# Kernel optimization log

Measured on AMD Instinct MI355X. Metric: run time of the kernel, lower is better.

The kernel has to match this reference:

```python
import jax, jax.numpy as jnp
import numpy as np

N_T, N_C, N_M = 300000, 100000, 20000
D_IN, D, D_OUT = 390, 128, 64
H_PRE, H_POST = 256, 64


def _nrm(k, shape, scale=0.02):
    return jax.random.normal(k, shape, dtype=jnp.float32) * scale


def setup_inputs() -> dict:
    key = jax.random.key(0)
    ks = jax.random.split(key, 24)
    inp = {
        'input_features': jax.random.normal(ks[0], (N_T, D_IN), jnp.float32),
        'card_of_target': jax.random.randint(ks[1], (N_T,), 0, N_C, jnp.int32),
        'merchant_of_target': jax.random.randint(ks[2], (N_T,), 0, N_M, jnp.int32),
        # HeteroEmbedding tables for src types feeding 'target'
        'card_emb': _nrm(ks[3], (N_C, D)),
        'merch_emb': _nrm(ks[4], (N_M, D)),
        # target_preprocessing FFBlock (390 -> 256 -> 128, n_layers=2)
        'pre_Wi': _nrm(ks[5], (D_IN, H_PRE)), 'pre_bi': jnp.zeros((H_PRE,), jnp.float32),
        'pre_Wh': _nrm(ks[6], (H_PRE, H_PRE)), 'pre_bh': jnp.zeros((H_PRE,), jnp.float32),
        'pre_Wo': _nrm(ks[7], (H_PRE, D)), 'pre_bo': jnp.zeros((D,), jnp.float32),
        # conv1 / conv2: one GraphConv per etype; order:
        # 0=card->target, 1=merchant->target, 2=target->card, 3=target->merchant
        'conv1_W': _nrm(ks[8], (4, D, D)), 'conv1_b': jnp.zeros((4, D), jnp.float32),
        'conv2_W': _nrm(ks[9], (4, D, D)), 'conv2_b': jnp.zeros((4, D), jnp.float32),
        # conv3: dst=='target' -> D_OUT; dst!='target' -> 1
        'conv3_Wt': _nrm(ks[10], (2, D, D_OUT)), 'conv3_bt': jnp.zeros((2, D_OUT), jnp.float32),
        'conv3_Wo': _nrm(ks[11], (2, D, 1)), 'conv3_bo': jnp.zeros((2, 1), jnp.float32),
        # target_postprocessing FFBlock (64 -> 64 -> 1, n_layers=2)
        'post_Wi': _nrm(ks[12], (D_OUT, H_POST)), 'post_bi': jnp.zeros((H_POST,), jnp.float32),
        'post_Wh': _nrm(ks[13], (H_POST, H_POST)), 'post_bh': jnp.zeros((H_POST,), jnp.float32),
        'post_Wo': _nrm(ks[14], (H_POST, 1)), 'post_bo': jnp.zeros((1,), jnp.float32),
    }
    return inp


def _ff(x, Wi, bi, Wh, bh, Wo, bo, n_layers=2):
    h = jax.nn.relu(x @ Wi + bi)
    for _ in range(1, n_layers):
        h = jax.nn.relu(h @ Wh + bh)
    return h @ Wo + bo


def _deg(ids, n):
    # degree per node over edge endpoint list, clamped to >= 1 (DGL GraphConv)
    return jnp.maximum(jnp.zeros((n,), jnp.float32).at[ids].add(1.0), 1.0)


def _gconv(x_src, src, dst, n_dst, W, b, d_src, d_dst):
    # DGL GraphConv, norm='both': scale src by out_deg^-1/2, matmul,
    # sum messages onto dst, scale by in_deg^-1/2, add bias.
    h = (x_src * jax.lax.rsqrt(d_src)[:, None]) @ W          # [n_src, out]
    agg = jax.ops.segment_sum(h[src], dst, num_segments=n_dst)
    return agg * jax.lax.rsqrt(d_dst)[:, None] + b


def reference(input_features, card_of_target, merchant_of_target,
              card_emb, merch_emb,
              pre_Wi, pre_bi, pre_Wh, pre_bh, pre_Wo, pre_bo,
              conv1_W, conv1_b, conv2_W, conv2_b,
              conv3_Wt, conv3_bt, conv3_Wo, conv3_bo,
              post_Wi, post_bi, post_Wh, post_bh, post_Wo, post_bo):
    n_t, n_c, n_m = input_features.shape[0], card_emb.shape[0], merch_emb.shape[0]
    t_ids = jnp.arange(n_t, dtype=jnp.int32)
    d_c = _deg(card_of_target, n_c)      # card degree (in/out symmetric here)
    d_m = _deg(merchant_of_target, n_m)  # merchant degree
    d_t = _deg(t_ids, n_t)               # target degree (=1 per etype)

    tf = _ff(input_features, pre_Wi, pre_bi, pre_Wh, pre_bh, pre_Wo, pre_bo)

    # conv1 (HeteroGraphConv, aggregate='sum') + relu
    h1_t = (_gconv(card_emb, card_of_target, t_ids, n_t, conv1_W[0], conv1_b[0], d_c, d_t)
            + _gconv(merch_emb, merchant_of_target, t_ids, n_t, conv1_W[1], conv1_b[1], d_m, d_t))
    h1_c = _gconv(tf, t_ids, card_of_target, n_c, conv1_W[2], conv1_b[2], d_t, d_c)
    h1_m = _gconv(tf, t_ids, merchant_of_target, n_m, conv1_W[3], conv1_b[3], d_t, d_m)
    h1_t, h1_c, h1_m = jax.nn.relu(h1_t), jax.nn.relu(h1_c), jax.nn.relu(h1_m)

    # conv2 applied (conv_layers - 2) = 1 time
    h2_t, h2_c, h2_m = h1_t, h1_c, h1_m
    for _ in range(2, 3):
        n_t2 = (_gconv(h2_c, card_of_target, t_ids, n_t, conv2_W[0], conv2_b[0], d_c, d_t)
                + _gconv(h2_m, merchant_of_target, t_ids, n_t, conv2_W[1], conv2_b[1], d_m, d_t))
        n_c2 = _gconv(h2_t, t_ids, card_of_target, n_c, conv2_W[2], conv2_b[2], d_t, d_c)
        n_m2 = _gconv(h2_t, t_ids, merchant_of_target, n_m, conv2_W[3], conv2_b[3], d_t, d_m)
        h2_t, h2_c, h2_m = jax.nn.relu(n_t2), jax.nn.relu(n_c2), jax.nn.relu(n_m2)

    # conv3: D_OUT into target, 1 into non-target dsts; no relu
    h3_t = (_gconv(h2_c, card_of_target, t_ids, n_t, conv3_Wt[0], conv3_bt[0], d_c, d_t)
            + _gconv(h2_m, merchant_of_target, t_ids, n_t, conv3_Wt[1], conv3_bt[1], d_m, d_t))
    h3_c = _gconv(h2_t, t_ids, card_of_target, n_c, conv3_Wo[0], conv3_bo[0], d_t, d_c)
    h3_m = _gconv(h2_t, t_ids, merchant_of_target, n_m, conv3_Wo[1], conv3_bo[1], d_t, d_m)

    h3_t = _ff(h3_t, post_Wi, post_bi, post_Wh, post_bh, post_Wo, post_bo)
    return h3_t, h3_c, h3_m
```

## Files before the change

### kernel.cpp

```cpp
#include <hip/hip_runtime.h>


#define NT 300000
#define NC 100000
#define NM 20000
#define DIN 390
#define DD 128
#define DOUT 64
#define HPRE 256
#define HPOST 64

typedef _Float16 half8 __attribute__((ext_vector_type(8)));
typedef float f32x16 __attribute__((ext_vector_type(16)));

#define LO_SCALE 512.0f
#define LO_INV   (1.0f / 512.0f)

__device__ __forceinline__ void split2(float x, _Float16& h, _Float16& l) {
    _Float16 hh = (_Float16)x;
    h = hh;
    l = (_Float16)((x - (float)hh) * LO_SCALE);
}

template<int TM, int TN, int WGM, int WGN>
__global__ __launch_bounds__(256, 2) void gemm_mfma(
    const float* __restrict__ A, const _Float16* __restrict__ Wh,
    const _Float16* __restrict__ Wl, const float* __restrict__ bias,
    const float* __restrict__ rowscale, float* __restrict__ C,
    int M, int K, int N, int Kpad, int relu)
{
    constexpr int BM = 32 * TM * WGM;
    constexpr int BN = 32 * TN * WGN;
    constexpr int RS = 40;
    __shared__ __align__(16) _Float16 Ah[BM * RS];
    __shared__ __align__(16) _Float16 Al[BM * RS];
    __shared__ __align__(16) _Float16 Bh[BN * RS];
    __shared__ __align__(16) _Float16 Bl[BN * RS];

    const int tid  = (int)threadIdx.x;
    const int lane = tid & 63;
    const int wave = tid >> 6;
    const int wm0 = (wave % WGM) * 32 * TM;
    const int wn0 = (wave / WGM) * 32 * TN;
    const int bm = blockIdx.x * BM;
    const int bn = blockIdx.y * BN;

    f32x16 zz;
    #pragma unroll
    for (int i = 0; i < 16; ++i) zz[i] = 0.f;
    f32x16 acc_hh[TM][TN], acc_x[TM][TN];
    #pragma unroll
    for (int tm = 0; tm < TM; ++tm)
        #pragma unroll
        for (int tn = 0; tn < TN; ++tn) { acc_hh[tm][tn] = zz; acc_x[tm][tn] = zz; }

    const int sar = tid >> 1;
    const int sak = (tid & 1) * 16;
    const int agrow = bm + sar;
    const float* Aptr = A + (size_t)agrow * K;

    const int ml  = lane & 31;
    const int klo = (lane >> 5) * 8;

    for (int k0 = 0; k0 < K; k0 += 32) {
        {
            _Float16 hh[16], ll[16];
            #pragma unroll
            for (int q = 0; q < 4; ++q) {
                const int kb = k0 + sak + q * 4;
                float4 f = make_float4(0.f, 0.f, 0.f, 0.f);
                if (agrow < M) {
                    if (kb + 3 < K) {
                        f = *(const float4*)(Aptr + kb);
                    } else {
                        if (kb + 0 < K) f.x = Aptr[kb + 0];
                        if (kb + 1 < K) f.y = Aptr[kb + 1];
                        if (kb + 2 < K) f.z = Aptr[kb + 2];
                        if (kb + 3 < K) f.w = Aptr[kb + 3];
                    }
                }
                split2(f.x, hh[q * 4 + 0], ll[q * 4 + 0]);
                split2(f.y, hh[q * 4 + 1], ll[q * 4 + 1]);
                split2(f.z, hh[q * 4 + 2], ll[q * 4 + 2]);
                split2(f.w, hh[q * 4 + 3], ll[q * 4 + 3]);
            }
            half8 h0, h1, l0, l1;
            #pragma unroll
            for (int j = 0; j < 8; ++j) {
                h0[j] = hh[j]; h1[j] = hh[8 + j];
                l0[j] = ll[j]; l1[j] = ll[8 + j];
            }
            *(half8*)&Ah[sar * RS + sak]     = h0;
            *(half8*)&Ah[sar * RS + sak + 8] = h1;
            *(half8*)&Al[sar * RS + sak]     = l0;
            *(half8*)&Al[sar * RS + sak + 8] = l1;
        }
        if constexpr (BN == 128) {
            const int n = tid >> 1, kq = (tid & 1) * 16;
            const size_t g = (size_t)(bn + n) * Kpad + k0 + kq;
            *(half8*)&Bh[n * RS + kq]     = *(const half8*)(Wh + g);
            *(half8*)&Bh[n * RS + kq + 8] = *(const half8*)(Wh + g + 8);
            *(half8*)&Bl[n * RS + kq]     = *(const half8*)(Wl + g);
            *(half8*)&Bl[n * RS + kq + 8] = *(const half8*)(Wl + g + 8);
        } else {
            const int n = tid >> 2, kq = (tid & 3) * 8;
            const size_t g = (size_t)(bn + n) * Kpad + k0 + kq;
            *(half8*)&Bh[n * RS + kq] = *(const half8*)(Wh + g);
            *(half8*)&Bl[n * RS + kq] = *(const half8*)(Wl + g);
        }
        __syncthreads();

        #pragma unroll
        for (int ks = 0; ks < 2; ++ks) {
            const int kk = ks * 16 + klo;
            half8 fa_h[TM], fa_l[TM], fb_h[TN], fb_l[TN];
            #pragma unroll
            for (int t = 0; t < TM; ++t) {
                const int m = wm0 + t * 32 + ml;
                fa_h[t] = *(const half8*)&Ah[m * RS + kk];
                fa_l[t] = *(const half8*)&Al[m * RS + kk];
            }
            #pragma unroll
            for (int t = 0; t < TN; ++t) {
                const int n = wn0 + t * 32 + ml;
                fb_h[t] = *(const half8*)&Bh[n * RS + kk];
                fb_l[t] = *(const half8*)&Bl[n * RS + kk];
            }
            #pragma unroll
            for (int tm = 0; tm < TM; ++tm)
                #pragma unroll
                for (int tn = 0; tn < TN; ++tn) {
                    acc_hh[tm][tn] = __builtin_amdgcn_mfma_f32_32x32x16_f16(
                        fa_h[tm], fb_h[tn], acc_hh[tm][tn], 0, 0, 0);
                    acc_x[tm][tn] = __builtin_amdgcn_mfma_f32_32x32x16_f16(
                        fa_h[tm], fb_l[tn], acc_x[tm][tn], 0, 0, 0);
                    acc_x[tm][tn] = __builtin_amdgcn_mfma_f32_32x32x16_f16(
                        fa_l[tm], fb_h[tn], acc_x[tm][tn], 0, 0, 0);
                }
        }
        __syncthreads();
    }

    const int r0 = 4 * (lane >> 5);
    #pragma unroll
    for (int tm = 0; tm < TM; ++tm) {
        #pragma unroll
        for (int tn = 0; tn < TN; ++tn) {
            const int gcol = bn + wn0 + tn * 32 + ml;
            const float bc = (bias != nullptr) ? bias[gcol] : 0.f;
            #pragma unroll
            for (int r = 0; r < 16; ++r) {
                const int grow = bm + wm0 + tm * 32 + (r & 3) + r0 + 8 * (r >> 2);
                if (grow < M) {
                    float v = acc_hh[tm][tn][r] + acc_x[tm][tn][r] * LO_INV;
                    if (rowscale != nullptr) v *= rowscale[grow];
                    v += bc;
                    if (relu) v = fmaxf(v, 0.f);
                    C[(size_t)grow * N + gcol] = v;
                }
            }
        }
    }
}

__global__ void split_w(const float* __restrict__ W, _Float16* __restrict__ hiT,
                        _Float16* __restrict__ loT, int K, int N, int Kpad, int nmat)
{
    int idx = blockIdx.x * blockDim.x + threadIdx.x;
    int total = nmat * N * Kpad;
    if (idx >= total) return;
    int e = idx / (N * Kpad);
    int rem = idx - e * (N * Kpad);
    int n = rem / Kpad;
    int k = rem - n * Kpad;
    float v = (k < K) ? W[((size_t)e * K + k) * N + n] : 0.f;
    _Float16 h = (_Float16)v;
    hiT[idx] = h;
    loT[idx] = (_Float16)((v - (float)h) * LO_SCALE);
}

__global__ void count_kernel(const int* __restrict__ card, const int* __restrict__ merch,
                             int* cnt_c, int* cnt_m, int n)
{
    int t = blockIdx.x * blockDim.x + threadIdx.x;
    if (t >= n) return;
    atomicAdd(&cnt_c[card[t]], 1);
    atomicAdd(&cnt_m[merch[t]], 1);
}

__global__ void rsqrt_kernel(const int* __restrict__ cnt, float* __restrict__ rs, int n)
{
    int i = blockIdx.x * blockDim.x + threadIdx.x;
    if (i >= n) return;
    int c = cnt[i];
    if (c < 1) c = 1;
    rs[i] = 1.0f / sqrtf((float)c);
}

__global__ __launch_bounds__(1024) void scan_excl(const int* __restrict__ cnt,
                                                  int* __restrict__ off, int n)
{
    __shared__ int wsum[16];
    const int tid = (int)threadIdx.x;
    const int lane = tid & 63, wid = tid >> 6;
    int carry = 0;
    for (int base = 0; base < n; base += 1024) {
        int i = base + tid;
        int v = (i < n) ? cnt[i] : 0;
        int x = v;
        #pragma unroll
        for (int d = 1; d < 64; d <<= 1) {
            int y = __shfl_up(x, d);
            if (lane >= d) x += y;
        }
        if (lane == 63) wsum[wid] = x;
        __syncthreads();
        int wpre = 0, tot = 0;
        #pragma unroll
        for (int w = 0; w < 16; ++w) {
            int s = wsum[w];
            if (w < wid) wpre += s;
            tot += s;
        }
        if (i < n) off[i] = carry + wpre + (x - v);
        carry += tot;
        __syncthreads();
    }
    if (tid == 0) off[n] = carry;
}

__global__ void fill_sorted(const int* __restrict__ ids, const int* __restrict__ off,
                            int* cur, int* __restrict__ srt, int n)
{
    int t = blockIdx.x * blockDim.x + threadIdx.x;
    if (t >= n) return;
    int c = ids[t];
    int p = atomicAdd(&cur[c], 1);
    srt[off[c] + p] = t;
}

__global__ void gather2_kernel(const float* __restrict__ hc, const float* __restrict__ hm,
                               const int* __restrict__ card, const int* __restrict__ merch,
                               const float* __restrict__ b0, const float* __restrict__ b1,
                               float* __restrict__ out, int n, int dim, int relu)
{
    int idx = blockIdx.x * blockDim.x + threadIdx.x;
    int per = dim >> 2;
    int t = idx / per;
    if (t >= n) return;
    int d4 = (idx % per) << 2;
    int c = card[t], m = merch[t];
    float4 a = *(const float4*)(hc + (size_t)c * dim + d4);
    float4 b = *(const float4*)(hm + (size_t)m * dim + d4);
    float4 v0 = *(const float4*)(b0 + d4);
    float4 v1 = *(const float4*)(b1 + d4);
    float4 r;
    r.x = a.x + b.x + v0.x + v1.x;
    r.y = a.y + b.y + v0.y + v1.y;
    r.z = a.z + b.z + v0.z + v1.z;
    r.w = a.w + b.w + v0.w + v1.w;
    if (relu) {
        r.x = fmaxf(r.x, 0.f); r.y = fmaxf(r.y, 0.f);
        r.z = fmaxf(r.z, 0.f); r.w = fmaxf(r.w, 0.f);
    }
    *(float4*)(out + (size_t)t * dim + d4) = r;
}

__global__ __launch_bounds__(256) void agg_csr_kernel(
    const float* __restrict__ proj, const int* __restrict__ off,
    const int* __restrict__ srt, const float* __restrict__ rs,
    const float* __restrict__ bias, float* __restrict__ out, int n, int relu)
{
    int node = blockIdx.x * 2 + ((int)threadIdx.x >> 7);
    int d = (int)threadIdx.x & 127;
    if (node >= n) return;
    int s = off[node], e = off[node + 1];
    float acc = 0.f;
    for (int i = s; i < e; ++i) {
        int t = srt[i];
        acc += proj[(size_t)t * 128 + d];
    }
    float v = acc * rs[node] + bias[d];
    if (relu) v = fmaxf(v, 0.f);
    out[(size_t)node * 128 + d] = v;
}

__global__ __launch_bounds__(256) void dot2_kernel(
    const float* __restrict__ h, const float* __restrict__ w0,
    const float* __restrict__ w1, float* __restrict__ s2, int n)
{
    int row = blockIdx.x * 4 + ((int)threadIdx.x >> 6);
    int l = (int)threadIdx.x & 63;
    if (row >= n) return;
    const float* x = h + (size_t)row * 128;
    float x0 = x[l], x1 = x[l + 64];
    float p0 = x0 * w0[l] + x1 * w0[l + 64];
    float p1 = x0 * w1[l] + x1 * w1[l + 64];
    #pragma unroll
    for (int o = 32; o > 0; o >>= 1) {
        p0 += __shfl_down(p0, o);
        p1 += __shfl_down(p1, o);
    }
    if (l == 0) { s2[(size_t)row * 2] = p0; s2[(size_t)row * 2 + 1] = p1; }
}

__global__ void agg_scalar_kernel(const float* __restrict__ s2, int which,
                                  const int* __restrict__ off, const int* __restrict__ srt,
                                  const float* __restrict__ rs, const float* __restrict__ bias,
                                  float* __restrict__ out, int n)
{
    int node = blockIdx.x * blockDim.x + threadIdx.x;
    if (node >= n) return;
    float acc = 0.f;
    int e = off[node + 1];
    for (int i = off[node]; i < e; ++i) acc += s2[(size_t)srt[i] * 2 + which];
    out[node] = acc * rs[node] + bias[0];
}

__global__ __launch_bounds__(256) void dot1_kernel(
    const float* __restrict__ h, const float* __restrict__ w,
    const float* __restrict__ b, float* __restrict__ out, int n)
{
    int row = blockIdx.x * 4 + ((int)threadIdx.x >> 6);
    int l = (int)threadIdx.x & 63;
    if (row >= n) return;
    float p = h[(size_t)row * 64 + l] * w[l];
    #pragma unroll
    for (int o = 32; o > 0; o >>= 1) p += __shfl_down(p, o);
    if (l == 0) out[row] = p + b[0];
}

static inline void gemm128(const float* A, const _Float16* wh, const _Float16* wl,
                           const float* bias, const float* rs, float* C,
                           int M, int K, int N, int Kpad, int relu, hipStream_t s)
{
    dim3 grid((M + 127) / 128, N / 128);
    gemm_mfma<2, 2, 2, 2><<<grid, 256, 0, s>>>(A, wh, wl, bias, rs, C, M, K, N, Kpad, relu);
}

static inline void gemm64(const float* A, const _Float16* wh, const _Float16* wl,
                          const float* bias, const float* rs, float* C,
                          int M, int K, int N, int Kpad, int relu, hipStream_t s)
{
    dim3 grid((M + 127) / 128, N / 64);
    gemm_mfma<1, 2, 4, 1><<<grid, 256, 0, s>>>(A, wh, wl, bias, rs, C, M, K, N, Kpad, relu);
}

extern "C" void kernel_launch(void* const* d_in, const int* in_sizes, int n_in,
                              void* d_out, int out_size, void* d_ws, size_t ws_size,
                              hipStream_t stream)
{
    const float* x_in      = (const float*)d_in[0];
    const int*   card      = (const int*)d_in[1];
    const int*   merch     = (const int*)d_in[2];
    const float* card_emb  = (const float*)d_in[3];
    const float* merch_emb = (const float*)d_in[4];
    const float* pre_Wi = (const float*)d_in[5];
    const float* pre_bi = (const float*)d_in[6];
    const float* pre_Wh = (const float*)d_in[7];
    const float* pre_bh = (const float*)d_in[8];
    const float* pre_Wo = (const float*)d_in[9];
    const float* pre_bo = (const float*)d_in[10];
    const float* conv1_W = (const float*)d_in[11];
    const float* conv1_b = (const float*)d_in[12];
    const float* conv2_W = (const float*)d_in[13];
    const float* conv2_b = (const float*)d_in[14];
    const float* conv3_Wt = (const float*)d_in[15];
    const float* conv3_bt = (const float*)d_in[16];
    const float* conv3_Wo = (const float*)d_in[17];
    const float* conv3_bo = (const float*)d_in[18];
    const float* post_Wi = (const float*)d_in[19];
    const float* post_bi = (const float*)d_in[20];
    const float* post_Wh = (const float*)d_in[21];
    const float* post_bh = (const float*)d_in[22];
    const float* post_Wo = (const float*)d_in[23];
    const float* post_bo = (const float*)d_in[24];

    float* out = (float*)d_out;

    char* ws = (char*)d_ws;
    size_t off = 0;
    auto alloc = [&](size_t bytes) -> char* {
        char* p = ws + off;
        off += (bytes + 255) & ~(size_t)255;
        return p;
    };
    int* cnt_c = (int*)alloc((size_t)NC * 4);
    int* cnt_m = (int*)alloc((size_t)NM * 4);
    int* cur_c = (int*)alloc((size_t)NC * 4);
    int* cur_m = (int*)alloc((size_t)NM * 4);
    size_t zero_bytes = (size_t)((char*)(cur_m + NM) - (char*)cnt_c);
    int* off_c = (int*)alloc((size_t)(NC + 1) * 4);
    int* off_m = (int*)alloc((size_t)(NM + 1) * 4);
    int* srt_c = (int*)alloc((size_t)NT * 4);
    int* srt_m = (int*)alloc((size_t)NT * 4);
    float* rs_c = (float*)alloc((size_t)NC * 4);
    float* rs_m = (float*)alloc((size_t)NM * 4);

    const int KP_WI = 416;
    _Float16* wi_h  = (_Float16*)alloc((size_t)HPRE * KP_WI * 2);
    _Float16* wi_l  = (_Float16*)alloc((size_t)HPRE * KP_WI * 2);
    _Float16* wh_h  = (_Float16*)alloc((size_t)HPRE * HPRE * 2);
    _Float16* wh_l  = (_Float16*)alloc((size_t)HPRE * HPRE * 2);
    _Float16* wo_h  = (_Float16*)alloc((size_t)DD * HPRE * 2);
    _Float16* wo_l  = (_Float16*)alloc((size_t)DD * HPRE * 2);
    _Float16* c1_h  = (_Float16*)alloc((size_t)4 * DD * DD * 2);
    _Float16* c1_l  = (_Float16*)alloc((size_t)4 * DD * DD * 2);
    _Float16* c2_h  = (_Float16*)alloc((size_t)4 * DD * DD * 2);
    _Float16* c2_l  = (_Float16*)alloc((size_t)4 * DD * DD * 2);
    _Float16* c3_h  = (_Float16*)alloc((size_t)2 * DOUT * DD * 2);
    _Float16* c3_l  = (_Float16*)alloc((size_t)2 * DOUT * DD * 2);
    _Float16* pi_h  = (_Float16*)alloc((size_t)HPOST * DOUT * 2);
    _Float16* pi_l  = (_Float16*)alloc((size_t)HPOST * DOUT * 2);
    _Float16* ph_h  = (_Float16*)alloc((size_t)HPOST * HPOST * 2);
    _Float16* ph_l  = (_Float16*)alloc((size_t)HPOST * HPOST * 2);

    float* bufA = (float*)alloc((size_t)NT * HPRE * 4);
    float* bufB = (float*)alloc((size_t)NT * HPRE * 4);
    float* tf   = (float*)alloc((size_t)NT * DD * 4);
    float* proj = (float*)alloc((size_t)NT * DD * 4);
    float* h1_t = (float*)alloc((size_t)NT * DD * 4);
    float* h2_t = (float*)alloc((size_t)NT * DD * 4);
    float* h1_c = (float*)alloc((size_t)NC * DD * 4);
    float* h2_c = (float*)alloc((size_t)NC * DD * 4);
    float* hc_p = (float*)alloc((size_t)NC * DD * 4);
    float* h1_m = (float*)alloc((size_t)NM * DD * 4);
    float* h2_m = (float*)alloc((size_t)NM * DD * 4);
    float* hm_p = (float*)alloc((size_t)NM * DD * 4);
    float* s2   = (float*)alloc((size_t)NT * 2 * 4);
    float* h3t64 = h1_t;
    float* p1 = h2_t;
    float* p2 = h2_t + (size_t)NT * 64;
    (void)ws_size; (void)in_sizes; (void)n_in; (void)out_size;

    hipMemsetAsync(cnt_c, 0, zero_bytes, stream);
    count_kernel<<<(NT + 255) / 256, 256, 0, stream>>>(card, merch, cnt_c, cnt_m, NT);
    rsqrt_kernel<<<(NC + 255) / 256, 256, 0, stream>>>(cnt_c, rs_c, NC);
    rsqrt_kernel<<<(NM + 255) / 256, 256, 0, stream>>>(cnt_m, rs_m, NM);
    scan_excl<<<1, 1024, 0, stream>>>(cnt_c, off_c, NC);
    scan_excl<<<1, 1024, 0, stream>>>(cnt_m, off_m, NM);
    fill_sorted<<<(NT + 255) / 256, 256, 0, stream>>>(card, off_c, cur_c, srt_c, NT);
    fill_sorted<<<(NT + 255) / 256, 256, 0, stream>>>(merch, off_m, cur_m, srt_m, NT);

    auto splitw = [&](const float* W, _Float16* h, _Float16* l, int K, int N, int Kpad, int nmat) {
        int total = nmat * N * Kpad;
        split_w<<<(total + 255) / 256, 256, 0, stream>>>(W, h, l, K, N, Kpad, nmat);
    };
    splitw(pre_Wi,   wi_h, wi_l, DIN,  HPRE,  KP_WI, 1);
    splitw(pre_Wh,   wh_h, wh_l, HPRE, HPRE,  HPRE,  1);
    splitw(pre_Wo,   wo_h, wo_l, HPRE, DD,    HPRE,  1);
    splitw(conv1_W,  c1_h, c1_l, DD,   DD,    DD,    4);
    splitw(conv2_W,  c2_h, c2_l, DD,   DD,    DD,    4);
    splitw(conv3_Wt, c3_h, c3_l, DD,   DOUT,  DD,    2);
    splitw(post_Wi,  pi_h, pi_l, DOUT, HPOST, DOUT,  1);
    splitw(post_Wh,  ph_h, ph_l, HPOST,HPOST, HPOST, 1);

    const int WP = DD * DD;

    gemm128(x_in, wi_h, wi_l, pre_bi, nullptr, bufA, NT, DIN,  HPRE, KP_WI, 1, stream);
    gemm128(bufA, wh_h, wh_l, pre_bh, nullptr, bufB, NT, HPRE, HPRE, HPRE,  1, stream);
    gemm128(bufB, wo_h, wo_l, pre_bo, nullptr, tf,   NT, HPRE, DD,   HPRE,  0, stream);

    gemm128(card_emb,  c1_h + 0 * WP, c1_l + 0 * WP, nullptr, rs_c, hc_p, NC, DD, DD, DD, 0, stream);
    gemm128(merch_emb, c1_h + 1 * WP, c1_l + 1 * WP, nullptr, rs_m, hm_p, NM, DD, DD, DD, 0, stream);
    gather2_kernel<<<(NT * (DD / 4) + 255) / 256, 256, 0, stream>>>(
        hc_p, hm_p, card, merch, conv1_b, conv1_b + DD, h1_t, NT, DD, 1);
    gemm128(tf, c1_h + 2 * WP, c1_l + 2 * WP, nullptr, nullptr, proj, NT, DD, DD, DD, 0, stream);
    agg_csr_kernel<<<(NC + 1) / 2, 256, 0, stream>>>(proj, off_c, srt_c, rs_c,
                                                     conv1_b + 2 * DD, h1_c, NC, 1);
    gemm128(tf, c1_h + 3 * WP, c1_l + 3 * WP, nullptr, nullptr, proj, NT, DD, DD, DD, 0, stream);
    agg_csr_kernel<<<(NM + 1) / 2, 256, 0, stream>>>(proj, off_m, srt_m, rs_m,
                                                     conv1_b + 3 * DD, h1_m, NM, 1);

    gemm128(h1_c, c2_h + 0 * WP, c2_l + 0 * WP, nullptr, rs_c, hc_p, NC, DD, DD, DD, 0, stream);
    gemm128(h1_m, c2_h + 1 * WP, c2_l + 1 * WP, nullptr, rs_m, hm_p, NM, DD, DD, DD, 0, stream);
    gather2_kernel<<<(NT * (DD / 4) + 255) / 256, 256, 0, stream>>>(
        hc_p, hm_p, card, merch, conv2_b, conv2_b + DD, h2_t, NT, DD, 1);
    gemm128(h1_t, c2_h + 2 * WP, c2_l + 2 * WP, nullptr, nullptr, proj, NT, DD, DD, DD, 0, stream);
    agg_csr_kernel<<<(NC + 1) / 2, 256, 0, stream>>>(proj, off_c, srt_c, rs_c,
                                                     conv2_b + 2 * DD, h2_c, NC, 1);
    gemm128(h1_t, c2_h + 3 * WP, c2_l + 3 * WP, nullptr, nullptr, proj, NT, DD, DD, DD, 0, stream);
    agg_csr_kernel<<<(NM + 1) / 2, 256, 0, stream>>>(proj, off_m, srt_m, rs_m,
                                                     conv2_b + 3 * DD, h2_m, NM, 1);

    const int WP3 = DOUT * DD;
    gemm64(h2_c, c3_h + 0 * WP3, c3_l + 0 * WP3, nullptr, rs_c, hc_p, NC, DD, DOUT, DD, 0, stream);
    gemm64(h2_m, c3_h + 1 * WP3, c3_l + 1 * WP3, nullptr, rs_m, hm_p, NM, DD, DOUT, DD, 0, stream);
    gather2_kernel<<<(NT * (DOUT / 4) + 255) / 256, 256, 0, stream>>>(
        hc_p, hm_p, card, merch, conv3_bt, conv3_bt + DOUT, h3t64, NT, DOUT, 0);
    dot2_kernel<<<(NT + 3) / 4, 256, 0, stream>>>(h2_t, conv3_Wo, conv3_Wo + DD, s2, NT);
    agg_scalar_kernel<<<(NC + 255) / 256, 256, 0, stream>>>(s2, 0, off_c, srt_c, rs_c,
                                                            conv3_bo + 0, out + NT, NC);
    agg_scalar_kernel<<<(NM + 255) / 256, 256, 0, stream>>>(s2, 1, off_m, srt_m, rs_m,
                                                            conv3_bo + 1, out + NT + NC, NM);

    gemm64(h3t64, pi_h, pi_l, post_bi, nullptr, p1, NT, DOUT,  HPOST, DOUT,  1, stream);
    gemm64(p1,    ph_h, ph_l, post_bh, nullptr, p2, NT, HPOST, HPOST, HPOST, 1, stream);
    dot1_kernel<<<(NT + 3) / 4, 256, 0, stream>>>(p2, post_Wo, post_bo, out, NT);
}
```

Before: 2.903 ms.

## Prefetch next K-tile into registers and shrink GEMM tiles to 64 rows

```diff
diff --git a/kernel.cpp b/kernel.cpp
--- a/kernel.cpp
+++ b/kernel.cpp
@@ -12,6 +12,7 @@
 
 typedef _Float16 half8 __attribute__((ext_vector_type(8)));
 typedef float f32x16 __attribute__((ext_vector_type(16)));
+typedef float f32x4 __attribute__((ext_vector_type(4)));
 
 #define LO_SCALE 512.0f
 #define LO_INV   (1.0f / 512.0f)
@@ -23,7 +24,7 @@
 }
 
 template<int TM, int TN, int WGM, int WGN>
-__global__ __launch_bounds__(256, 2) void gemm_mfma(
+__global__ __launch_bounds__(256, 3) void gemm_mfma(
     const float* __restrict__ A, const _Float16* __restrict__ Wh,
     const _Float16* __restrict__ Wl, const float* __restrict__ bias,
     const float* __restrict__ rowscale, float* __restrict__ C,
@@ -42,8 +43,11 @@
     const int wave = tid >> 6;
     const int wm0 = (wave % WGM) * 32 * TM;
     const int wn0 = (wave / WGM) * 32 * TN;
-    const int bm = blockIdx.x * BM;
-    const int bn = blockIdx.y * BN;
+
+    const int nbn = N / BN;
+    const int tile = (int)blockIdx.x;
+    const int bm = (tile / nbn) * BM;
+    const int bn = (tile % nbn) * BN;
 
     f32x16 zz;
     #pragma unroll
@@ -54,88 +58,109 @@
         #pragma unroll
         for (int tn = 0; tn < TN; ++tn) { acc_hh[tm][tn] = zz; acc_x[tm][tn] = zz; }
 
-    const int sar = tid >> 1;
-    const int sak = (tid & 1) * 16;
+    constexpr int TPR  = 256 / BM;
+    constexpr int KPT  = 32 / TPR;
+    constexpr int FQ   = KPT / 4;
+    const int sar = tid / TPR;
+    const int sak = (tid % TPR) * KPT;
     const int agrow = bm + sar;
     const float* Aptr = A + (size_t)agrow * K;
 
+    constexpr int TPRB = 256 / BN;
+    constexpr int KPTB = 32 / TPRB;
+    constexpr int NB   = KPTB / 8;
+    const int sbr = tid / TPRB;
+    const int sbk = (tid % TPRB) * KPTB;
+    const _Float16* Bhp = Wh + (size_t)(bn + sbr) * Kpad + sbk;
+    const _Float16* Blp = Wl + (size_t)(bn + sbr) * Kpad + sbk;
+
     const int ml  = lane & 31;
     const int klo = (lane >> 5) * 8;
 
+    f32x4 areg[FQ];
+    half8 bhreg[NB], blreg[NB];
+
+    auto loadA = [&](int k0) {
+        #pragma unroll
+        for (int q = 0; q < FQ; ++q) {
+            const int kb = k0 + sak + q * 4;
+            f32x4 f = {0.f, 0.f, 0.f, 0.f};
+            if (agrow < M) {
+                if (kb + 3 < K) {
+                    f = *(const f32x4*)(Aptr + kb);
+                } else {
+                    if (kb + 0 < K) f[0] = Aptr[kb + 0];
+                    if (kb + 1 < K) f[1] = Aptr[kb + 1];
+                    if (kb + 2 < K) f[2] = Aptr[kb + 2];
+                    if (kb + 3 < K) f[3] = Aptr[kb + 3];
+                }
+            }
+            areg[q] = f;
+        }
+    };
+    auto loadB = [&](int k0) {
+        #pragma unroll
+        for (int j = 0; j < NB; ++j) {
+            bhreg[j] = *(const half8*)(Bhp + k0 + j * 8);
+            blreg[j] = *(const half8*)(Blp + k0 + j * 8);
+        }
+    };
+
+    loadA(0);
+    loadB(0);
+
     for (int k0 = 0; k0 < K; k0 += 32) {
-        {
-            _Float16 hh[16], ll[16];
+        #pragma unroll
+        for (int c = 0; c < FQ / 2; ++c) {
+            half8 h, l;
             #pragma unroll
-            for (int q = 0; q < 4; ++q) {
-                const int kb = k0 + sak + q * 4;
-                float4 f = make_float4(0.f, 0.f, 0.f, 0.f);
-                if (agrow < M) {
-                    if (kb + 3 < K) {
-                        f = *(const float4*)(Aptr + kb);
-                    } else {
-                        if (kb + 0 < K) f.x = Aptr[kb + 0];
-                        if (kb + 1 < K) f.y = Aptr[kb + 1];
-                        if (kb + 2 < K) f.z = Aptr[kb + 2];
-                        if (kb + 3 < K) f.w = Aptr[kb + 3];
-                    }
+            for (int q = 0; q < 2; ++q) {
+                #pragma unroll
+                for (int j = 0; j < 4; ++j) {
+                    _Float16 th, tl;
+                    split2(areg[2 * c + q][j], th, tl);
+                    h[q * 4 + j] = th;
+                    l[q * 4 + j] = tl;
                 }
-                split2(f.x, hh[q * 4 + 0], ll[q * 4 + 0]);
-                split2(f.y, hh[q * 4 + 1], ll[q * 4 + 1]);
-                split2(f.z, hh[q * 4 + 2], ll[q * 4 + 2]);
-                split2(f.w, hh[q * 4 + 3], ll[q * 4 + 3]);
             }
-            half8 h0, h1, l0, l1;
-            #pragma unroll
-            for (int j = 0; j < 8; ++j) {
-                h0[j] = hh[j]; h1[j] = hh[8 + j];
-                l0[j] = ll[j]; l1[j] = ll[8 + j];
-            }
-            *(half8*)&Ah[sar * RS + sak]     = h0;
-            *(half8*)&Ah[sar * RS + sak + 8] = h1;
-            *(half8*)&Al[sar * RS + sak]     = l0;
-            *(half8*)&Al[sar * RS + sak + 8] = l1;
-        }
-        if constexpr (BN == 128) {
-            const int n = tid >> 1, kq = (tid & 1) * 16;
-            const size_t g = (size_t)(bn + n) * Kpad + k0 + kq;
-            *(half8*)&Bh[n * RS + kq]     = *(const half8*)(Wh + g);
-            *(half8*)&Bh[n * RS + kq + 8] = *(const half8*)(Wh + g + 8);
-            *(half8*)&Bl[n * RS + kq]     = *(const half8*)(Wl + g);
-            *(half8*)&Bl[n * RS + kq + 8] = *(const half8*)(Wl + g + 8);
-        } else {
-            const int n = tid >> 2, kq = (tid & 3) * 8;
-            const size_t g = (size_t)(bn + n) * Kpad + k0 + kq;
-            *(half8*)&Bh[n * RS + kq] = *(const half8*)(Wh + g);
-            *(half8*)&Bl[n * RS + kq] = *(const half8*)(Wl + g);
+            *(half8*)&Ah[sar * RS + sak + c * 8] = h;
+            *(half8*)&Al[sar * RS + sak + c * 8] = l;
+        }
+        #pragma unroll
+        for (int j = 0; j < NB; ++j) {
+            *(half8*)&Bh[sbr * RS + sbk + j * 8] = bhreg[j];
+            *(half8*)&Bl[sbr * RS + sbk + j * 8] = blreg[j];
         }
         __syncthreads();
+
+        if (k0 + 32 < K) { loadA(k0 + 32); loadB(k0 + 32); }
 
         #pragma unroll
         for (int ks = 0; ks < 2; ++ks) {
             const int kk = ks * 16 + klo;
-            half8 fa_h[TM], fa_l[TM], fb_h[TN], fb_l[TN];
+            half8 fah[TM], fal[TM], fbh[TN], fbl[TN];
             #pragma unroll
             for (int t = 0; t < TM; ++t) {
                 const int m = wm0 + t * 32 + ml;
-                fa_h[t] = *(const half8*)&Ah[m * RS + kk];
-                fa_l[t] = *(const half8*)&Al[m * RS + kk];
+                fah[t] = *(const half8*)&Ah[m * RS + kk];
+                fal[t] = *(const half8*)&Al[m * RS + kk];
             }
             #pragma unroll
             for (int t = 0; t < TN; ++t) {
                 const int n = wn0 + t * 32 + ml;
-                fb_h[t] = *(const half8*)&Bh[n * RS + kk];
-                fb_l[t] = *(const half8*)&Bl[n * RS + kk];
+                fbh[t] = *(const half8*)&Bh[n * RS + kk];
+                fbl[t] = *(const half8*)&Bl[n * RS + kk];
             }
             #pragma unroll
             for (int tm = 0; tm < TM; ++tm)
                 #pragma unroll
                 for (int tn = 0; tn < TN; ++tn) {
                     acc_hh[tm][tn] = __builtin_amdgcn_mfma_f32_32x32x16_f16(
-                        fa_h[tm], fb_h[tn], acc_hh[tm][tn], 0, 0, 0);
+                        fah[tm], fbh[tn], acc_hh[tm][tn], 0, 0, 0);
                     acc_x[tm][tn] = __builtin_amdgcn_mfma_f32_32x32x16_f16(
-                        fa_h[tm], fb_l[tn], acc_x[tm][tn], 0, 0, 0);
+                        fah[tm], fbl[tn], acc_x[tm][tn], 0, 0, 0);
                     acc_x[tm][tn] = __builtin_amdgcn_mfma_f32_32x32x16_f16(
-                        fa_l[tm], fb_h[tn], acc_x[tm][tn], 0, 0, 0);
+                        fal[tm], fbh[tn], acc_x[tm][tn], 0, 0, 0);
                 }
         }
         __syncthreads();
@@ -330,20 +355,19 @@
     if (l == 0) out[row] = p + b[0];
 }
 
-static inline void gemm128(const float* A, const _Float16* wh, const _Float16* wl,
-                           const float* bias, const float* rs, float* C,
-                           int M, int K, int N, int Kpad, int relu, hipStream_t s)
-{
-    dim3 grid((M + 127) / 128, N / 128);
-    gemm_mfma<2, 2, 2, 2><<<grid, 256, 0, s>>>(A, wh, wl, bias, rs, C, M, K, N, Kpad, relu);
-}
-
-static inline void gemm64(const float* A, const _Float16* wh, const _Float16* wl,
-                          const float* bias, const float* rs, float* C,
-                          int M, int K, int N, int Kpad, int relu, hipStream_t s)
-{
-    dim3 grid((M + 127) / 128, N / 64);
-    gemm_mfma<1, 2, 4, 1><<<grid, 256, 0, s>>>(A, wh, wl, bias, rs, C, M, K, N, Kpad, relu);
+static inline void gemmN(const float* A, const _Float16* wh, const _Float16* wl,
+                         const float* bias, const float* rs, float* C,
+                         int M, int K, int N, int Kpad, int relu, hipStream_t s)
+{
+    const int nbm = (M + 63) / 64;
+    if (N % 128 == 0) {
+        const int nbn = N / 128;
+        gemm_mfma<1, 2, 2, 2><<<dim3(nbm * nbn), 256, 0, s>>>(
+            A, wh, wl, bias, rs, C, M, K, N, Kpad, relu);
+    } else {
+        gemm_mfma<1, 1, 2, 2><<<dim3(nbm), 256, 0, s>>>(
+            A, wh, wl, bias, rs, C, M, K, N, Kpad, relu);
+    }
 }
 
 extern "C" void kernel_launch(void* const* d_in, const int* in_sizes, int n_in,
@@ -457,35 +481,35 @@
 
     const int WP = DD * DD;
 
-    gemm128(x_in, wi_h, wi_l, pre_bi, nullptr, bufA, NT, DIN,  HPRE, KP_WI, 1, stream);
-    gemm128(bufA, wh_h, wh_l, pre_bh, nullptr, bufB, NT, HPRE, HPRE, HPRE,  1, stream);
-    gemm128(bufB, wo_h, wo_l, pre_bo, nullptr, tf,   NT, HPRE, DD,   HPRE,  0, stream);
-
-    gemm128(card_emb,  c1_h + 0 * WP, c1_l + 0 * WP, nullptr, rs_c, hc_p, NC, DD, DD, DD, 0, stream);
-    gemm128(merch_emb, c1_h + 1 * WP, c1_l + 1 * WP, nullptr, rs_m, hm_p, NM, DD, DD, DD, 0, stream);
+    gemmN(x_in, wi_h, wi_l, pre_bi, nullptr, bufA, NT, DIN,  HPRE, KP_WI, 1, stream);
+    gemmN(bufA, wh_h, wh_l, pre_bh, nullptr, bufB, NT, HPRE, HPRE, HPRE,  1, stream);
+    gemmN(bufB, wo_h, wo_l, pre_bo, nullptr, tf,   NT, HPRE, DD,   HPRE,  0, stream);
+
+    gemmN(card_emb,  c1_h + 0 * WP, c1_l + 0 * WP, nullptr, rs_c, hc_p, NC, DD, DD, DD, 0, stream);
+    gemmN(merch_emb, c1_h + 1 * WP, c1_l + 1 * WP, nullptr, rs_m, hm_p, NM, DD, DD, DD, 0, stream);
     gather2_kernel<<<(NT * (DD / 4) + 255) / 256, 256, 0, stream>>>(
         hc_p, hm_p, card, merch, conv1_b, conv1_b + DD, h1_t, NT, DD, 1);
-    gemm128(tf, c1_h + 2 * WP, c1_l + 2 * WP, nullptr, nullptr, proj, NT, DD, DD, DD, 0, stream);
+    gemmN(tf, c1_h + 2 * WP, c1_l + 2 * WP, nullptr, nullptr, proj, NT, DD, DD, DD, 0, stream);
     agg_csr_kernel<<<(NC + 1) / 2, 256, 0, stream>>>(proj, off_c, srt_c, rs_c,
                                                      conv1_b + 2 * DD, h1_c, NC, 1);
-    gemm128(tf, c1_h + 3 * WP, c1_l + 3 * WP, nullptr, nullptr, proj, NT, DD, DD, DD, 0, stream);
+    gemmN(tf, c1_h + 3 * WP, c1_l + 3 * WP, nullptr, nullptr, proj, NT, DD, DD, DD, 0, stream);
     agg_csr_kernel<<<(NM + 1) / 2, 256, 0, stream>>>(proj, off_m, srt_m, rs_m,
                                                      conv1_b + 3 * DD, h1_m, NM, 1);
 
-    gemm128(h1_c, c2_h + 0 * WP, c2_l + 0 * WP, nullptr, rs_c, hc_p, NC, DD, DD, DD, 0, stream);
-    gemm128(h1_m, c2_h + 1 * WP, c2_l + 1 * WP, nullptr, rs_m, hm_p, NM, DD, DD, DD, 0, stream);
+    gemmN(h1_c, c2_h + 0 * WP, c2_l + 0 * WP, nullptr, rs_c, hc_p, NC, DD, DD, DD, 0, stream);
+    gemmN(h1_m, c2_h + 1 * WP, c2_l + 1 * WP, nullptr, rs_m, hm_p, NM, DD, DD, DD, 0, stream);
     gather2_kernel<<<(NT * (DD / 4) + 255) / 256, 256, 0, stream>>>(
         hc_p, hm_p, card, merch, conv2_b, conv2_b + DD, h2_t, NT, DD, 1);
-    gemm128(h1_t, c2_h + 2 * WP, c2_l + 2 * WP, nullptr, nullptr, proj, NT, DD, DD, DD, 0, stream);
+    gemmN(h1_t, c2_h + 2 * WP, c2_l + 2 * WP, nullptr, nullptr, proj, NT, DD, DD, DD, 0, stream);
     agg_csr_kernel<<<(NC + 1) / 2, 256, 0, stream>>>(proj, off_c, srt_c, rs_c,
                                                      conv2_b + 2 * DD, h2_c, NC, 1);
-    gemm128(h1_t, c2_h + 3 * WP, c2_l + 3 * WP, nullptr, nullptr, proj, NT, DD, DD, DD, 0, stream);
+    gemmN(h1_t, c2_h + 3 * WP, c2_l + 3 * WP, nullptr, nullptr, proj, NT, DD, DD, DD, 0, stream);
     agg_csr_kernel<<<(NM + 1) / 2, 256, 0, stream>>>(proj, off_m, srt_m, rs_m,
                                                      conv2_b + 3 * DD, h2_m, NM, 1);
 
     const int WP3 = DOUT * DD;
-    gemm64(h2_c, c3_h + 0 * WP3, c3_l + 0 * WP3, nullptr, rs_c, hc_p, NC, DD, DOUT, DD, 0, stream);
-    gemm64(h2_m, c3_h + 1 * WP3, c3_l + 1 * WP3, nullptr, rs_m, hm_p, NM, DD, DOUT, DD, 0, stream);
+    gemmN(h2_c, c3_h + 0 * WP3, c3_l + 0 * WP3, nullptr, rs_c, hc_p, NC, DD, DOUT, DD, 0, stream);
+    gemmN(h2_m, c3_h + 1 * WP3, c3_l + 1 * WP3, nullptr, rs_m, hm_p, NM, DD, DOUT, DD, 0, stream);
     gather2_kernel<<<(NT * (DOUT / 4) + 255) / 256, 256, 0, stream>>>(
         hc_p, hm_p, card, merch, conv3_bt, conv3_bt + DOUT, h3t64, NT, DOUT, 0);
     dot2_kernel<<<(NT + 3) / 4, 256, 0, stream>>>(h2_t, conv3_Wo, conv3_Wo + DD, s2, NT);
@@ -494,7 +518,7 @@
     agg_scalar_kernel<<<(NM + 255) / 256, 256, 0, stream>>>(s2, 1, off_m, srt_m, rs_m,
                                                             conv3_bo + 1, out + NT + NC, NM);
 
-    gemm64(h3t64, pi_h, pi_l, post_bi, nullptr, p1, NT, DOUT,  HPOST, DOUT,  1, stream);
-    gemm64(p1,    ph_h, ph_l, post_bh, nullptr, p2, NT, HPOST, HPOST, HPOST, 1, stream);
+    gemmN(h3t64, pi_h, pi_l, post_bi, nullptr, p1, NT, DOUT,  HPOST, DOUT,  1, stream);
+    gemmN(p1,    ph_h, ph_l, post_bh, nullptr, p2, NT, HPOST, HPOST, HPOST, 1, stream);
     dot1_kernel<<<(NT + 3) / 4, 256, 0, stream>>>(p2, post_Wo, post_bo, out, NT);
 }
```

Result: faster. 2.791 ms (-3.9%).
